# Kernel tuning notes

Hardware: AMD Instinct MI355X
Metric: run time of the kernel (lower is better)

## Reference

```python
import jax, jax.numpy as jnp
import numpy as np

GROUPS = 32
EPS = 1e-6


def group_norm(x, gamma, beta):
    # x: [b, c, d, h, w]
    b, c, d, h, w = x.shape
    xg = x.reshape(b, GROUPS, c // GROUPS, d, h, w)
    mean = xg.mean(axis=(2, 3, 4, 5), keepdims=True)
    var = xg.var(axis=(2, 3, 4, 5), keepdims=True)
    xn = ((xg - mean) * jax.lax.rsqrt(var + EPS)).reshape(b, c, d, h, w)
    return xn * gamma[None, :, None, None, None] + beta[None, :, None, None, None]


def conv1x1(x, w, bias):
    # 1x1x1 Conv3d == channel matmul. x: [b,c,d,h,w], w: [out,in]
    return jnp.einsum('bcdhw,oc->bodhw', x, w) + bias[None, :, None, None, None]


def setup_inputs() -> dict:
    key = jax.random.key(0)
    ks = jax.random.split(key, 6)
    C = 256
    x = jax.random.normal(ks[0], (4, C, 16, 16, 16), dtype=jnp.float32)
    s = 1.0 / np.sqrt(C)
    return {
        'x': x,
        'gn_gamma': jnp.ones((C,), jnp.float32),
        'gn_beta': jnp.zeros((C,), jnp.float32),
        'wq': jax.random.normal(ks[1], (C, C), jnp.float32) * s,
        'bq': jnp.zeros((C,), jnp.float32),
        'wk': jax.random.normal(ks[2], (C, C), jnp.float32) * s,
        'bk': jnp.zeros((C,), jnp.float32),
        'wv': jax.random.normal(ks[3], (C, C), jnp.float32) * s,
        'bv': jnp.zeros((C,), jnp.float32),
        'wo': jax.random.normal(ks[4], (C, C), jnp.float32) * s,
        'bo': jnp.zeros((C,), jnp.float32),
    }


def reference(x, gn_gamma, gn_beta, wq, bq, wk, bk, wv, bv, wo, bo):
    b, c, d, h, w = x.shape
    n = d * h * w
    hn = group_norm(x, gn_gamma, gn_beta)
    q = conv1x1(hn, wq, bq).reshape(b, c, n)  # [b,c,n]
    k = conv1x1(hn, wk, bk).reshape(b, c, n)
    v = conv1x1(hn, wv, bv).reshape(b, c, n)
    # NOTE: no 1/sqrt(c) scaling, faithful to source
    scores = jnp.einsum('bci,bcj->bij', q, k)          # [b,n,n]
    attn = jax.nn.softmax(scores, axis=-1)
    out = jnp.einsum('bij,bcj->bci', attn, v)           # [b,c,n]
    out = out.reshape(b, c, d, h, w)
    out = conv1x1(out, wo, bo)
    return x + out
```

## Files before the change

kernel.cpp:

```cpp
#include <hip/hip_runtime.h>
#include <hip/hip_bf16.h>

#define C_ 256
#define N_ 4096
#define B_ 4
#define NG_ 32
#define CPG_ 8
#define SPLITS 4
#define JT_PER (N_ / 32 / SPLITS)

typedef _Float16 f16;
typedef __attribute__((ext_vector_type(8))) _Float16 f16v8;
typedef __attribute__((ext_vector_type(2))) __fp16 fp16v2;
typedef __attribute__((ext_vector_type(4))) float f32x4;

__device__ __forceinline__ f16v8 ldh(const f16* p) {
    return *reinterpret_cast<const f16v8*>(p);
}
__device__ __forceinline__ f32x4 mfma16(f16v8 a, f16v8 b, f32x4 c) {
    return __builtin_amdgcn_mfma_f32_16x16x32_f16(a, b, c, 0, 0, 0);
}
__device__ __forceinline__ unsigned int pkh(float a, float b) {
    fp16v2 t = __builtin_amdgcn_cvt_pkrtz(a, b);
    return __builtin_bit_cast(unsigned int, t);
}

__global__ __launch_bounds__(256) void conv_w_kernel(
    const float* __restrict__ wq, const float* __restrict__ wk,
    const float* __restrict__ wv, const float* __restrict__ wo,
    f16* __restrict__ wq16, f16* __restrict__ wk16,
    f16* __restrict__ wv16, f16* __restrict__ wo16)
{
    int idx = blockIdx.x * 256 + threadIdx.x;
    wq16[idx] = (f16)wq[idx];
    wk16[idx] = (f16)wk[idx];
    wv16[idx] = (f16)wv[idx];
    wo16[idx] = (f16)wo[idx];
}

__global__ __launch_bounds__(256) void gn_kernel(
    const float* __restrict__ x, const float* __restrict__ gamma,
    const float* __restrict__ beta, f16* __restrict__ hn)
{
    int b = blockIdx.x >> 5, g = blockIdx.x & 31;
    const float* xp = x + (size_t)(b * C_ + g * CPG_) * N_;
    int tid = threadIdx.x;
    float s = 0.f, s2 = 0.f;
    for (int idx = tid; idx < CPG_ * N_; idx += 256) {
        float v = xp[idx];
        s += v; s2 += v * v;
    }
    #pragma unroll
    for (int off = 32; off > 0; off >>= 1) {
        s  += __shfl_down(s, off);
        s2 += __shfl_down(s2, off);
    }
    __shared__ float rs[4], rs2[4], stat[2];
    if ((tid & 63) == 0) { rs[tid >> 6] = s; rs2[tid >> 6] = s2; }
    __syncthreads();
    if (tid == 0) {
        float S  = rs[0] + rs[1] + rs[2] + rs[3];
        float S2 = rs2[0] + rs2[1] + rs2[2] + rs2[3];
        float mean = S / (float)(CPG_ * N_);
        float var  = S2 / (float)(CPG_ * N_) - mean * mean;
        stat[0] = mean;
        stat[1] = rsqrtf(var + 1e-6f);
    }
    __syncthreads();
    float mean = stat[0], rstd = stat[1];
    float ga[CPG_], be[CPG_];
    #pragma unroll
    for (int cc = 0; cc < CPG_; cc++) {
        ga[cc] = gamma[g * CPG_ + cc] * rstd;
        be[cc] = beta[g * CPG_ + cc];
    }
    for (int i = tid; i < N_; i += 256) {
        f16v8 H;
        #pragma unroll
        for (int cc = 0; cc < CPG_; cc++)
            H[cc] = (f16)((xp[(size_t)cc * N_ + i] - mean) * ga[cc] + be[cc]);
        *reinterpret_cast<f16v8*>(hn + (size_t)(b * N_ + i) * C_ + g * CPG_) = H;
    }
}

__global__ __launch_bounds__(256) void proj_qk_kernel(
    const f16* __restrict__ hn, const f16* __restrict__ wq16,
    const f16* __restrict__ wk16, const float* __restrict__ bq,
    const float* __restrict__ bk, f16* __restrict__ qo, f16* __restrict__ ko)
{
    int it = blockIdx.x, b = blockIdx.y, which = blockIdx.z;
    const f16* wgt = which ? wk16 : wq16;
    const float* bias = which ? bk : bq;
    f16* outp = which ? ko : qo;
    int tid = threadIdx.x, w = tid >> 6, l = tid & 63;
    int l15 = l & 15, lhi = l >> 4;
    int i0 = it * 64 + w * 16;
    size_t arow = (size_t)(b * N_ + i0 + l15) * C_ + lhi * 8;
    f16v8 af[8];
    #pragma unroll
    for (int kk = 0; kk < 8; kk++) af[kk] = ldh(hn + arow + kk * 32);
    for (int oc = 0; oc < 16; oc++) {
        f32x4 acc = {0.f, 0.f, 0.f, 0.f};
        size_t wrow = (size_t)(oc * 16 + l15) * C_ + lhi * 8;
        #pragma unroll
        for (int kk = 0; kk < 8; kk++)
            acc = mfma16(af[kk], ldh(wgt + wrow + kk * 32), acc);
        float bia = bias[oc * 16 + l15];
        #pragma unroll
        for (int r = 0; r < 4; r++)
            outp[(size_t)(b * N_ + i0 + lhi * 4 + r) * C_ + oc * 16 + l15] =
                (f16)(acc[r] + bia);
    }
}

__global__ __launch_bounds__(256) void proj_v_kernel(
    const f16* __restrict__ hn, const f16* __restrict__ wv16,
    const float* __restrict__ bv, f16* __restrict__ vT)
{
    int it = blockIdx.x, b = blockIdx.y;
    int tid = threadIdx.x, w = tid >> 6, l = tid & 63;
    int l15 = l & 15, lhi = l >> 4;
    int o0 = w * 64, i0 = it * 64;
    f32x4 acc[4][4];
    #pragma unroll
    for (int mc = 0; mc < 4; mc++)
        #pragma unroll
        for (int nc = 0; nc < 4; nc++) acc[mc][nc] = (f32x4){0.f, 0.f, 0.f, 0.f};
    for (int kk = 0; kk < 8; kk++) {
        f16v8 af[4], bfv[4];
        #pragma unroll
        for (int mc = 0; mc < 4; mc++)
            af[mc] = ldh(wv16 + (size_t)(o0 + mc * 16 + l15) * C_ + kk * 32 + lhi * 8);
        #pragma unroll
        for (int nc = 0; nc < 4; nc++)
            bfv[nc] = ldh(hn + (size_t)(b * N_ + i0 + nc * 16 + l15) * C_ + kk * 32 + lhi * 8);
        #pragma unroll
        for (int mc = 0; mc < 4; mc++)
            #pragma unroll
            for (int nc = 0; nc < 4; nc++)
                acc[mc][nc] = mfma16(af[mc], bfv[nc], acc[mc][nc]);
    }
    #pragma unroll
    for (int mc = 0; mc < 4; mc++) {
        float bia[4];
        #pragma unroll
        for (int r = 0; r < 4; r++) bia[r] = bv[o0 + mc * 16 + lhi * 4 + r];
        #pragma unroll
        for (int nc = 0; nc < 4; nc++)
            #pragma unroll
            for (int r = 0; r < 4; r++) {
                int o = o0 + mc * 16 + lhi * 4 + r;
                int i = i0 + nc * 16 + l15;
                vT[(size_t)(b * C_ + o) * N_ + i] = (f16)(acc[mc][nc][r] + bia[r]);
            }
    }
}

__device__ __forceinline__ void stage_k(const f16* kbase, f16* dst, int j0,
                                        int w, int l) {
    #pragma unroll
    for (int rd = 0; rd < 4; rd++) {
        int cb = (rd * 4 + w) * 64;
        int mc = cb + l;
        int row = mc >> 5;
        int xoff = ((mc & 31) << 4) ^ ((row & 7) << 4);
        const f16* gsrc = kbase + (size_t)(j0 + row) * C_ + (xoff >> 1);
        __builtin_amdgcn_global_load_lds(
            (const __attribute__((address_space(1))) void*)gsrc,
            (__attribute__((address_space(3))) void*)(dst + (size_t)cb * 8),
            16, 0, 0);
    }
}
__device__ __forceinline__ void stage_v(const f16* vbase, f16* dst, int j0,
                                        int w, int l) {
    int tid = w * 64 + l;
    int colu = ((l & 3) ^ ((l >> 3) & 3)) * 8;
    #pragma unroll
    for (int s = 0; s < 4; s++) {
        int cb = s * 256 + w * 64;
        const f16* gsrc = vbase + (size_t)(s * 64 + (tid >> 2)) * N_ + j0 + colu;
        __builtin_amdgcn_global_load_lds(
            (const __attribute__((address_space(1))) void*)gsrc,
            (__attribute__((address_space(3))) void*)(dst + (size_t)cb * 8),
            16, 0, 0);
    }
}

__global__ __launch_bounds__(256, 2) void flash_split_kernel(
    const f16* __restrict__ q, const f16* __restrict__ k,
    const f16* __restrict__ vT,
    f16* __restrict__ o0p, f16* __restrict__ o1p,
    f16* __restrict__ o2p, f16* __restrict__ o3p,
    float2* __restrict__ stats)
{
    int bi = blockIdx.x;
    int g = bi & 15;
    int it = bi >> 4;
    int b = g >> 2, split = g & 3;
    int tid = threadIdx.x, w = tid >> 6, l = tid & 63;
    int l15 = l & 15, lhi = l >> 4;
    int i0 = it * 128 + w * 32;
    int jt0 = split * JT_PER;
    __shared__ __align__(16) f16 kb[2][32][256];
    __shared__ __align__(16) f16 vb[2][256][32];
    __shared__ __align__(16) unsigned int Plds[4][2][16][20];

    const f16* kbase = k + (size_t)b * N_ * C_;
    const f16* vbase = vT + (size_t)b * C_ * N_;

    f16v8 qfA[8], qfB_[8];
    {
        size_t qrow0 = (size_t)(b * N_ + i0 + l15) * C_ + lhi * 8;
        size_t qrow1 = (size_t)(b * N_ + i0 + 16 + l15) * C_ + lhi * 8;
        #pragma unroll
        for (int kk = 0; kk < 8; kk++) {
            qfA[kk]  = ldh(q + qrow0 + kk * 32);
            qfB_[kk] = ldh(q + qrow1 + kk * 32);
        }
    }

    f32x4 oaccA[16], oaccB[16];
    #pragma unroll
    for (int cc = 0; cc < 16; cc++) {
        oaccA[cc] = (f32x4){0.f, 0.f, 0.f, 0.f};
        oaccB[cc] = (f32x4){0.f, 0.f, 0.f, 0.f};
    }
    float mA = -1e30f, rsA = 0.f;
    float mB = -1e30f, rsB = 0.f;

    int lhiV = lhi ^ ((l15 >> 1) & 3);

    stage_k(kbase, &kb[0][0][0], jt0 * 32, w, l);
    stage_v(vbase, &vb[0][0][0], jt0 * 32, w, l);
    __syncthreads();

    for (int jt = 0; jt < JT_PER; jt++) {
        int cur = jt & 1;
        int j0 = (jt0 + jt) * 32;

        if (jt + 1 < JT_PER) {
            stage_k(kbase, &kb[cur ^ 1][0][0], j0 + 32, w, l);
            stage_v(vbase, &vb[cur ^ 1][0][0], j0 + 32, w, l);
        }

        const char* kbc = (const char*)&kb[cur][0][0];
        f32x4 sA0 = {0.f,0.f,0.f,0.f}, sA1 = {0.f,0.f,0.f,0.f};
        f32x4 sB0 = {0.f,0.f,0.f,0.f}, sB1 = {0.f,0.f,0.f,0.f};
        #pragma unroll
        for (int kk = 0; kk < 8; kk++) {
            int row0 = l15, row1 = 16 + l15;
            int off0 = row0 * 512 + ((kk * 64 + lhi * 16) ^ ((row0 & 7) << 4));
            int off1 = row1 * 512 + ((kk * 64 + lhi * 16) ^ ((row1 & 7) << 4));
            f16v8 kf0 = *reinterpret_cast<const f16v8*>(kbc + off0);
            f16v8 kf1 = *reinterpret_cast<const f16v8*>(kbc + off1);
            sA0 = mfma16(kf0, qfA[kk], sA0);
            sA1 = mfma16(kf1, qfA[kk], sA1);
            sB0 = mfma16(kf0, qfB_[kk], sB0);
            sB1 = mfma16(kf1, qfB_[kk], sB1);
        }

        float mtA = fmaxf(fmaxf(fmaxf(sA0[0], sA0[1]), fmaxf(sA0[2], sA0[3])),
                          fmaxf(fmaxf(sA1[0], sA1[1]), fmaxf(sA1[2], sA1[3])));
        float mtB = fmaxf(fmaxf(fmaxf(sB0[0], sB0[1]), fmaxf(sB0[2], sB0[3])),
                          fmaxf(fmaxf(sB1[0], sB1[1]), fmaxf(sB1[2], sB1[3])));
        mtA = fmaxf(mtA, __shfl_xor(mtA, 16));
        mtA = fmaxf(mtA, __shfl_xor(mtA, 32));
        mtB = fmaxf(mtB, __shfl_xor(mtB, 16));
        mtB = fmaxf(mtB, __shfl_xor(mtB, 32));
        if (!__all(mtA <= mA + 8.f && mtB <= mB + 8.f)) {
            float mnA = fmaxf(mA, mtA), mnB = fmaxf(mB, mtB);
            float scA = __expf(mA - mnA), scB = __expf(mB - mnB);
            mA = mnA; mB = mnB;
            rsA *= scA; rsB *= scB;
            #pragma unroll
            for (int cc = 0; cc < 16; cc++) {
                #pragma unroll
                for (int r = 0; r < 4; r++) {
                    oaccA[cc][r] *= scA;
                    oaccB[cc][r] *= scB;
                }
            }
        }
        float pA0[4], pA1[4], pB0[4], pB1[4];
        float lsA = 0.f, lsB = 0.f;
        #pragma unroll
        for (int r = 0; r < 4; r++) {
            pA0[r] = __expf(sA0[r] - mA);
            pA1[r] = __expf(sA1[r] - mA);
            pB0[r] = __expf(sB0[r] - mB);
            pB1[r] = __expf(sB1[r] - mB);
            lsA += pA0[r] + pA1[r];
            lsB += pB0[r] + pB1[r];
        }
        rsA += lsA; rsB += lsB;

        {
            uint2 pa = {pkh(pA0[0], pA0[1]), pkh(pA0[2], pA0[3])};
            uint2 pb = {pkh(pA1[0], pA1[1]), pkh(pA1[2], pA1[3])};
            *reinterpret_cast<uint2*>(&Plds[w][0][l15][lhi * 2])     = pa;
            *reinterpret_cast<uint2*>(&Plds[w][0][l15][8 + lhi * 2]) = pb;
            uint2 pc = {pkh(pB0[0], pB0[1]), pkh(pB0[2], pB0[3])};
            uint2 pd = {pkh(pB1[0], pB1[1]), pkh(pB1[2], pB1[3])};
            *reinterpret_cast<uint2*>(&Plds[w][1][l15][lhi * 2])     = pc;
            *reinterpret_cast<uint2*>(&Plds[w][1][l15][8 + lhi * 2]) = pd;
        }
        f16v8 pfA = *reinterpret_cast<const f16v8*>(&Plds[w][0][l15][lhi * 4]);
        f16v8 pfB = *reinterpret_cast<const f16v8*>(&Plds[w][1][l15][lhi * 4]);

        const f16* vbc = &vb[cur][0][0];
        #pragma unroll
        for (int cc = 0; cc < 16; cc++) {
            f16v8 vf = ldh(vbc + (cc * 16 + l15) * 32 + lhiV * 8);
            oaccA[cc] = mfma16(vf, pfA, oaccA[cc]);
            oaccB[cc] = mfma16(vf, pfB, oaccB[cc]);
        }

        __syncthreads();
    }

    rsA += __shfl_xor(rsA, 16); rsA += __shfl_xor(rsA, 32);
    rsB += __shfl_xor(rsB, 16); rsB += __shfl_xor(rsB, 32);
    float invA = 1.f / rsA, invB = 1.f / rsB;

    f16* op = (split == 0) ? o0p : (split == 1) ? o1p : (split == 2) ? o2p : o3p;
    size_t obaseA = (size_t)(b * N_ + i0 + l15) * C_;
    size_t obaseB = (size_t)(b * N_ + i0 + 16 + l15) * C_;
    #pragma unroll
    for (int cc = 0; cc < 16; cc++) {
        uint2 stA = {pkh(oaccA[cc][0] * invA, oaccA[cc][1] * invA),
                     pkh(oaccA[cc][2] * invA, oaccA[cc][3] * invA)};
        uint2 stB = {pkh(oaccB[cc][0] * invB, oaccB[cc][1] * invB),
                     pkh(oaccB[cc][2] * invB, oaccB[cc][3] * invB)};
        *reinterpret_cast<uint2*>(op + obaseA + cc * 16 + lhi * 4) = stA;
        *reinterpret_cast<uint2*>(op + obaseB + cc * 16 + lhi * 4) = stB;
    }
    if (lhi == 0) {
        stats[((size_t)split * B_ + b) * N_ + i0 + l15]      = make_float2(mA, rsA);
        stats[((size_t)split * B_ + b) * N_ + i0 + 16 + l15] = make_float2(mB, rsB);
    }
}

__global__ __launch_bounds__(256) void combine_kernel(
    const f16* __restrict__ o0p, const f16* __restrict__ o1p,
    const f16* __restrict__ o2p, const f16* __restrict__ o3p,
    const float2* __restrict__ stats, f16* __restrict__ att)
{
    int idx = blockIdx.x * 256 + threadIdx.x;
    int rowg = idx >> 5;
    int cof = (idx & 31) * 8;
    float2 st[SPLITS];
    float M = -1e30f;
    #pragma unroll
    for (int s = 0; s < SPLITS; s++) {
        st[s] = stats[(size_t)s * B_ * N_ + rowg];
        M = fmaxf(M, st[s].x);
    }
    float a[SPLITS], L = 0.f;
    #pragma unroll
    for (int s = 0; s < SPLITS; s++) {
        a[s] = st[s].y * __expf(st[s].x - M);
        L += a[s];
    }
    float inv = 1.f / L;
    size_t base = (size_t)rowg * C_ + cof;
    f16v8 v0 = ldh(o0p + base), v1 = ldh(o1p + base);
    f16v8 v2 = ldh(o2p + base), v3 = ldh(o3p + base);
    f16v8 o = v0 * (f16)(a[0] * inv) + v1 * (f16)(a[1] * inv)
            + v2 * (f16)(a[2] * inv) + v3 * (f16)(a[3] * inv);
    *reinterpret_cast<f16v8*>(att + base) = o;
}

__global__ __launch_bounds__(256) void final_kernel(
    const f16* __restrict__ att, const f16* __restrict__ wo16,
    const float* __restrict__ bo, const float* __restrict__ x,
    float* __restrict__ out)
{
    int bx = blockIdx.x, b = blockIdx.y;
    int it = bx >> 1, half = bx & 1;
    int tid = threadIdx.x, w = tid >> 6, l = tid & 63;
    int l15 = l & 15, lhi = l >> 4;
    int o0 = half * 128 + w * 32, i0 = it * 64;
    f32x4 acc[2][4];
    #pragma unroll
    for (int mc = 0; mc < 2; mc++)
        #pragma unroll
        for (int nc = 0; nc < 4; nc++) acc[mc][nc] = (f32x4){0.f, 0.f, 0.f, 0.f};
    for (int kk = 0; kk < 8; kk++) {
        f16v8 af[2], bfv[4];
        #pragma unroll
        for (int mc = 0; mc < 2; mc++)
            af[mc] = ldh(wo16 + (size_t)(o0 + mc * 16 + l15) * C_ + kk * 32 + lhi * 8);
        #pragma unroll
        for (int nc = 0; nc < 4; nc++)
            bfv[nc] = ldh(att + (size_t)(b * N_ + i0 + nc * 16 + l15) * C_ + kk * 32 + lhi * 8);
        #pragma unroll
        for (int mc = 0; mc < 2; mc++)
            #pragma unroll
            for (int nc = 0; nc < 4; nc++)
                acc[mc][nc] = mfma16(af[mc], bfv[nc], acc[mc][nc]);
    }
    #pragma unroll
    for (int mc = 0; mc < 2; mc++) {
        float bia[4];
        #pragma unroll
        for (int r = 0; r < 4; r++) bia[r] = bo[o0 + mc * 16 + lhi * 4 + r];
        #pragma unroll
        for (int nc = 0; nc < 4; nc++)
            #pragma unroll
            for (int r = 0; r < 4; r++) {
                int o = o0 + mc * 16 + lhi * 4 + r;
                int i = i0 + nc * 16 + l15;
                size_t idx = (size_t)(b * C_ + o) * N_ + i;
                out[idx] = x[idx] + acc[mc][nc][r] + bia[r];
            }
    }
}

extern "C" void kernel_launch(void* const* d_in, const int* in_sizes, int n_in,
                              void* d_out, int out_size, void* d_ws, size_t ws_size,
                              hipStream_t stream) {
    const float* x  = (const float*)d_in[0];
    const float* gg = (const float*)d_in[1];
    const float* gb = (const float*)d_in[2];
    const float* wq = (const float*)d_in[3];
    const float* bq = (const float*)d_in[4];
    const float* wk = (const float*)d_in[5];
    const float* bk = (const float*)d_in[6];
    const float* wv = (const float*)d_in[7];
    const float* bv = (const float*)d_in[8];
    const float* wo = (const float*)d_in[9];
    const float* bo = (const float*)d_in[10];
    float* out = (float*)d_out;

    char* p = (char*)d_ws;
    const size_t WSZ = (size_t)C_ * C_ * 2;
    const size_t HSZ = (size_t)B_ * N_ * C_ * 2;
    const size_t HN  = (size_t)B_ * N_ * C_;
    f16* wq16 = (f16*)p; p += WSZ;
    f16* wk16 = (f16*)p; p += WSZ;
    f16* wv16 = (f16*)p; p += WSZ;
    f16* wo16 = (f16*)p; p += WSZ;
    f16* hn   = (f16*)p; p += HSZ;
    f16* qo   = (f16*)p; p += HSZ;
    f16* ko   = (f16*)p; p += HSZ;
    f16* vt   = (f16*)p; p += HSZ;
    f16* oex  = (f16*)p; p += 3 * HSZ;
    float2* stats = (float2*)p; p += (size_t)SPLITS * B_ * N_ * sizeof(float2);

    f16* o0p = hn;
    f16* o1p = oex;
    f16* o2p = oex + HN;
    f16* o3p = oex + 2 * HN;
    f16* att = qo;

    conv_w_kernel<<<dim3(C_ * C_ / 256), 256, 0, stream>>>(
        wq, wk, wv, wo, wq16, wk16, wv16, wo16);
    gn_kernel<<<dim3(B_ * NG_), 256, 0, stream>>>(x, gg, gb, hn);
    proj_qk_kernel<<<dim3(N_ / 64, B_, 2), 256, 0, stream>>>(
        hn, wq16, wk16, bq, bk, qo, ko);
    proj_v_kernel<<<dim3(N_ / 64, B_), 256, 0, stream>>>(hn, wv16, bv, vt);
    flash_split_kernel<<<dim3(N_ / 128 * B_ * SPLITS), 256, 0, stream>>>(
        qo, ko, vt, o0p, o1p, o2p, o3p, stats);
    combine_kernel<<<dim3((int)(HN / 8 / 256)), 256, 0, stream>>>(
        o0p, o1p, o2p, o3p, stats, att);
    final_kernel<<<dim3(N_ / 64 * 2, B_), 256, 0, stream>>>(
        att, wo16, bo, x, out);
}
```

Before: 217.0 us.

## Split group norm into parallel stats/apply kernels and widen projection grids

Group norm moves from one block per (batch, group) to a partial-sum stats kernel with eight parts per group plus a separate apply kernel with many more blocks. The stats pass also uses float4 loads. The Q/K projection grid is split over output-channel halves and the V projection tile is halved, both to launch more blocks on the GPU. The flash kernel gets s_setprio hints around its MFMA loops. The cost is an extra kernel launch, a small partial-sum buffer, and more redundant A-fragment loads in the projections.

```diff
diff --git a/kernel.cpp b/kernel.cpp
--- a/kernel.cpp
+++ b/kernel.cpp
@@ -7,6 +7,7 @@
 #define NG_ 32
 #define CPG_ 8
 #define SPLITS 4
+#define GPARTS 8
 #define JT_PER (N_ / 32 / SPLITS)
 
 typedef _Float16 f16;
@@ -38,49 +39,62 @@
     wo16[idx] = (f16)wo[idx];
 }
 
-__global__ __launch_bounds__(256) void gn_kernel(
-    const float* __restrict__ x, const float* __restrict__ gamma,
-    const float* __restrict__ beta, f16* __restrict__ hn)
-{
-    int b = blockIdx.x >> 5, g = blockIdx.x & 31;
-    const float* xp = x + (size_t)(b * C_ + g * CPG_) * N_;
+__global__ __launch_bounds__(256) void gn_stats_kernel(
+    const float* __restrict__ x, float2* __restrict__ psums)
+{
+    int idx = blockIdx.x;
+    int part = idx & (GPARTS - 1);
+    int bg = idx >> 3;
+    const float4* xv = (const float4*)(x + (size_t)bg * (CPG_ * N_)
+                                         + (size_t)part * (CPG_ * N_ / GPARTS));
     int tid = threadIdx.x;
     float s = 0.f, s2 = 0.f;
-    for (int idx = tid; idx < CPG_ * N_; idx += 256) {
-        float v = xp[idx];
-        s += v; s2 += v * v;
+    #pragma unroll
+    for (int i = 0; i < CPG_ * N_ / GPARTS / 4 / 256; i++) {
+        float4 v = xv[i * 256 + tid];
+        s  += v.x + v.y + v.z + v.w;
+        s2 += v.x * v.x + v.y * v.y + v.z * v.z + v.w * v.w;
     }
     #pragma unroll
     for (int off = 32; off > 0; off >>= 1) {
         s  += __shfl_down(s, off);
         s2 += __shfl_down(s2, off);
     }
-    __shared__ float rs[4], rs2[4], stat[2];
+    __shared__ float rs[4], rs2[4];
     if ((tid & 63) == 0) { rs[tid >> 6] = s; rs2[tid >> 6] = s2; }
     __syncthreads();
-    if (tid == 0) {
-        float S  = rs[0] + rs[1] + rs[2] + rs[3];
-        float S2 = rs2[0] + rs2[1] + rs2[2] + rs2[3];
-        float mean = S / (float)(CPG_ * N_);
-        float var  = S2 / (float)(CPG_ * N_) - mean * mean;
-        stat[0] = mean;
-        stat[1] = rsqrtf(var + 1e-6f);
-    }
-    __syncthreads();
-    float mean = stat[0], rstd = stat[1];
-    float ga[CPG_], be[CPG_];
+    if (tid == 0)
+        psums[idx] = make_float2(rs[0] + rs[1] + rs[2] + rs[3],
+                                 rs2[0] + rs2[1] + rs2[2] + rs2[3]);
+}
+
+__global__ __launch_bounds__(256) void gn_apply_kernel(
+    const float* __restrict__ x, const float2* __restrict__ psums,
+    const float* __restrict__ gamma, const float* __restrict__ beta,
+    f16* __restrict__ hn)
+{
+    int idx = blockIdx.x;
+    int p2 = idx & 15;
+    int bg = idx >> 4;
+    int b = bg >> 5, g = bg & 31;
+    float S = 0.f, S2 = 0.f;
+    #pragma unroll
+    for (int s = 0; s < GPARTS; s++) {
+        float2 ps = psums[bg * GPARTS + s];
+        S += ps.x; S2 += ps.y;
+    }
+    float mean = S / (float)(CPG_ * N_);
+    float rstd = rsqrtf(S2 / (float)(CPG_ * N_) - mean * mean + 1e-6f);
+    int i = p2 * 256 + threadIdx.x;
+    const float* xp = x + (size_t)(b * C_ + g * CPG_) * N_;
+    f16v8 H;
     #pragma unroll
     for (int cc = 0; cc < CPG_; cc++) {
-        ga[cc] = gamma[g * CPG_ + cc] * rstd;
-        be[cc] = beta[g * CPG_ + cc];
-    }
-    for (int i = tid; i < N_; i += 256) {
-        f16v8 H;
-        #pragma unroll
-        for (int cc = 0; cc < CPG_; cc++)
-            H[cc] = (f16)((xp[(size_t)cc * N_ + i] - mean) * ga[cc] + be[cc]);
-        *reinterpret_cast<f16v8*>(hn + (size_t)(b * N_ + i) * C_ + g * CPG_) = H;
-    }
+        float ga = gamma[g * CPG_ + cc] * rstd;
+        float be = beta[g * CPG_ + cc];
+        H[cc] = (f16)((xp[(size_t)cc * N_ + i] - mean) * ga + be);
+    }
+    *reinterpret_cast<f16v8*>(hn + (size_t)(b * N_ + i) * C_ + g * CPG_) = H;
 }
 
 __global__ __launch_bounds__(256) void proj_qk_kernel(
@@ -88,7 +102,8 @@
     const f16* __restrict__ wk16, const float* __restrict__ bq,
     const float* __restrict__ bk, f16* __restrict__ qo, f16* __restrict__ ko)
 {
-    int it = blockIdx.x, b = blockIdx.y, which = blockIdx.z;
+    int it = blockIdx.x, b = blockIdx.y, z = blockIdx.z;
+    int which = z >> 1, ochalf = z & 1;
     const f16* wgt = which ? wk16 : wq16;
     const float* bias = which ? bk : bq;
     f16* outp = which ? ko : qo;
@@ -99,7 +114,7 @@
     f16v8 af[8];
     #pragma unroll
     for (int kk = 0; kk < 8; kk++) af[kk] = ldh(hn + arow + kk * 32);
-    for (int oc = 0; oc < 16; oc++) {
+    for (int oc = ochalf * 8; oc < ochalf * 8 + 8; oc++) {
         f32x4 acc = {0.f, 0.f, 0.f, 0.f};
         size_t wrow = (size_t)(oc * 16 + l15) * C_ + lhi * 8;
         #pragma unroll
@@ -120,24 +135,24 @@
     int it = blockIdx.x, b = blockIdx.y;
     int tid = threadIdx.x, w = tid >> 6, l = tid & 63;
     int l15 = l & 15, lhi = l >> 4;
-    int o0 = w * 64, i0 = it * 64;
-    f32x4 acc[4][4];
+    int o0 = w * 64, i0 = it * 32;
+    f32x4 acc[4][2];
     #pragma unroll
     for (int mc = 0; mc < 4; mc++)
         #pragma unroll
-        for (int nc = 0; nc < 4; nc++) acc[mc][nc] = (f32x4){0.f, 0.f, 0.f, 0.f};
+        for (int nc = 0; nc < 2; nc++) acc[mc][nc] = (f32x4){0.f, 0.f, 0.f, 0.f};
     for (int kk = 0; kk < 8; kk++) {
-        f16v8 af[4], bfv[4];
+        f16v8 af[4], bfv[2];
         #pragma unroll
         for (int mc = 0; mc < 4; mc++)
             af[mc] = ldh(wv16 + (size_t)(o0 + mc * 16 + l15) * C_ + kk * 32 + lhi * 8);
         #pragma unroll
-        for (int nc = 0; nc < 4; nc++)
+        for (int nc = 0; nc < 2; nc++)
             bfv[nc] = ldh(hn + (size_t)(b * N_ + i0 + nc * 16 + l15) * C_ + kk * 32 + lhi * 8);
         #pragma unroll
         for (int mc = 0; mc < 4; mc++)
             #pragma unroll
-            for (int nc = 0; nc < 4; nc++)
+            for (int nc = 0; nc < 2; nc++)
                 acc[mc][nc] = mfma16(af[mc], bfv[nc], acc[mc][nc]);
     }
     #pragma unroll
@@ -146,7 +161,7 @@
         #pragma unroll
         for (int r = 0; r < 4; r++) bia[r] = bv[o0 + mc * 16 + lhi * 4 + r];
         #pragma unroll
-        for (int nc = 0; nc < 4; nc++)
+        for (int nc = 0; nc < 2; nc++)
             #pragma unroll
             for (int r = 0; r < 4; r++) {
                 int o = o0 + mc * 16 + lhi * 4 + r;
@@ -246,6 +261,7 @@
         const char* kbc = (const char*)&kb[cur][0][0];
         f32x4 sA0 = {0.f,0.f,0.f,0.f}, sA1 = {0.f,0.f,0.f,0.f};
         f32x4 sB0 = {0.f,0.f,0.f,0.f}, sB1 = {0.f,0.f,0.f,0.f};
+        __builtin_amdgcn_s_setprio(1);
         #pragma unroll
         for (int kk = 0; kk < 8; kk++) {
             int row0 = l15, row1 = 16 + l15;
@@ -258,6 +274,7 @@
             sB0 = mfma16(kf0, qfB_[kk], sB0);
             sB1 = mfma16(kf1, qfB_[kk], sB1);
         }
+        __builtin_amdgcn_s_setprio(0);
 
         float mtA = fmaxf(fmaxf(fmaxf(sA0[0], sA0[1]), fmaxf(sA0[2], sA0[3])),
                           fmaxf(fmaxf(sA1[0], sA1[1]), fmaxf(sA1[2], sA1[3])));
@@ -308,12 +325,14 @@
         f16v8 pfB = *reinterpret_cast<const f16v8*>(&Plds[w][1][l15][lhi * 4]);
 
         const f16* vbc = &vb[cur][0][0];
+        __builtin_amdgcn_s_setprio(1);
         #pragma unroll
         for (int cc = 0; cc < 16; cc++) {
             f16v8 vf = ldh(vbc + (cc * 16 + l15) * 32 + lhiV * 8);
             oaccA[cc] = mfma16(vf, pfA, oaccA[cc]);
             oaccB[cc] = mfma16(vf, pfB, oaccB[cc]);
         }
+        __builtin_amdgcn_s_setprio(0);
 
         __syncthreads();
     }
@@ -446,6 +465,7 @@
     f16* vt   = (f16*)p; p += HSZ;
     f16* oex  = (f16*)p; p += 3 * HSZ;
     float2* stats = (float2*)p; p += (size_t)SPLITS * B_ * N_ * sizeof(float2);
+    float2* psums = (float2*)p; p += (size_t)B_ * NG_ * GPARTS * sizeof(float2);
 
     f16* o0p = hn;
     f16* o1p = oex;
@@ -455,10 +475,12 @@
 
     conv_w_kernel<<<dim3(C_ * C_ / 256), 256, 0, stream>>>(
         wq, wk, wv, wo, wq16, wk16, wv16, wo16);
-    gn_kernel<<<dim3(B_ * NG_), 256, 0, stream>>>(x, gg, gb, hn);
-    proj_qk_kernel<<<dim3(N_ / 64, B_, 2), 256, 0, stream>>>(
+    gn_stats_kernel<<<dim3(B_ * NG_ * GPARTS), 256, 0, stream>>>(x, psums);
+    gn_apply_kernel<<<dim3(B_ * NG_ * 16), 256, 0, stream>>>(
+        x, psums, gg, gb, hn);
+    proj_qk_kernel<<<dim3(N_ / 64, B_, 4), 256, 0, stream>>>(
         hn, wq16, wk16, bq, bk, qo, ko);
-    proj_v_kernel<<<dim3(N_ / 64, B_), 256, 0, stream>>>(hn, wv16, bv, vt);
+    proj_v_kernel<<<dim3(N_ / 32, B_), 256, 0, stream>>>(hn, wv16, bv, vt);
     flash_split_kernel<<<dim3(N_ / 128 * B_ * SPLITS), 256, 0, stream>>>(
         qo, ko, vt, o0p, o1p, o2p, o3p, stats);
     combine_kernel<<<dim3((int)(HN / 8 / 256)), 256, 0, stream>>>(
```

Result: faster. 185.4 us (-14.6%).
